# Optimization experiments

Measured on AMD Instinct MI355X. Metric: run time of the kernel, lower is better.

The kernel has to match this reference:

```python
import jax, jax.numpy as jnp
import numpy as np
import math

D_MODEL = 1024
D_ATTN = 128
D_MID = 128
L = 4096

def setup_inputs() -> dict:
    key = jax.random.key(0)
    ks = jax.random.split(key, 5)
    scale = 1.0 / math.sqrt(D_MODEL)
    return {
        "x": jax.random.normal(ks[0], (L, D_MODEL), jnp.float32),
        "z": jax.random.normal(ks[1], (L, D_MODEL), jnp.float32),
        "Wq": jax.random.normal(ks[2], (D_MODEL, D_ATTN), jnp.float32) * scale,
        "bq": jnp.zeros((D_ATTN,), jnp.float32),
        "Wk": jax.random.normal(ks[3], (D_MODEL, D_ATTN), jnp.float32) * scale,
        "bk": jnp.zeros((D_ATTN,), jnp.float32),
        "Wv": jax.random.normal(ks[4], (D_MODEL, D_MID), jnp.float32) * scale,
        "bv": jnp.zeros((D_MID,), jnp.float32),
    }

def reference(x, z, Wq, bq, Wk, bk, Wv, bv):
    # q: [L_x, d_attn], k: [L_z, d_attn], v: [L_z, d_mid]
    q = x @ Wq + bq
    k = z @ Wk + bk
    v = z @ Wv + bv
    inv_sqrt_d = 1.0 / math.sqrt(D_ATTN)
    s = (q @ k.T) * inv_sqrt_d            # [L_x, L_z]
    y = jax.nn.softmax(s, axis=-1) @ v    # [L_x, d_mid]
    return y
```

## Files before the change

kernel.cpp:

```cpp
#include <hip/hip_runtime.h>
#include <hip/hip_bf16.h>

typedef __attribute__((ext_vector_type(8))) short short8;
typedef __attribute__((ext_vector_type(4))) float f32x4;
typedef __attribute__((ext_vector_type(8))) _Float16 half8;

#define L_SEQ 4096
#define DM    1024
#define DA    128
#define AZ    16

#define OFF_QB  786432
#define OFF_KF  1835008
#define OFF_VF  2883584
#define OFF_OA  4063232
#define OA_BYTES ((size_t)AZ * L_SEQ * DA * 2)

__device__ __forceinline__ short f2bf(float f) {
    union { float f; unsigned u; } v; v.f = f;
    unsigned u = v.u;
    u += 0x7FFFu + ((u >> 16) & 1u);
    return (short)(u >> 16);
}

__device__ __forceinline__ unsigned cvt_pk_bf16(float lo, float hi) {
    unsigned r;
    asm("v_cvt_pk_bf16_f32 %0, %1, %2" : "=v"(r) : "v"(lo), "v"(hi));
    return r;
}

typedef const __attribute__((address_space(1))) void g_void_t;
typedef __attribute__((address_space(3))) void l_void_t;
__device__ __forceinline__ void g2lds16(const void* g, void* l) {
    __builtin_amdgcn_global_load_lds((g_void_t*)g, (l_void_t*)l, 16, 0, 0);
}

__global__ __launch_bounds__(256) void prep_w_kernel(
    const float* __restrict__ Wq, const float* __restrict__ Wk,
    const float* __restrict__ Wv, short8* __restrict__ WTf)
{
    const int m = blockIdx.y, kidx = blockIdx.x;
    const float* __restrict__ W = (m == 0) ? Wq : (m == 1) ? Wk : Wv;
    __shared__ __align__(16) float Ws[32 * 132];
    const int t = threadIdx.x;
#pragma unroll
    for (int i = 0; i < 4; i++) {
        const int u = i * 256 + t;
        const int kk = u >> 5, n4 = (u & 31) * 4;
        *(f32x4*)&Ws[kk * 132 + n4] = *(const f32x4*)&W[(size_t)(kidx * 32 + kk) * DA + n4];
    }
    __syncthreads();
#pragma unroll
    for (int i = 0; i < 2; i++) {
        const int u = i * 256 + t;
        const int nt = u >> 6, lane = u & 63, l16 = lane & 15, quad = lane >> 4;
        short8 fr;
#pragma unroll
        for (int j = 0; j < 8; j++)
            fr[j] = f2bf(Ws[(quad * 8 + j) * 132 + nt * 16 + l16]);
        WTf[((size_t)(m * 32 + kidx) * 8 + nt) * 64 + lane] = fr;
    }
}

__global__ __launch_bounds__(256, 1) void qkv_kernel(
    const float* __restrict__ x, const float* __restrict__ z,
    const char* __restrict__ WTraw,
    const float* __restrict__ bq, const float* __restrict__ bk,
    const float* __restrict__ bv,
    short* __restrict__ qb, short8* __restrict__ kf, short8* __restrict__ vf)
{
    __shared__ __align__(16) char smem[2][32768];

    const int t = threadIdx.x;
    const int wave = t >> 6, lane = t & 63;
    const int l16 = lane & 15, quad = lane >> 4;
    const int mtile = wave >> 1, nhalf = wave & 1;
    const int isKV = blockIdx.y;
    const int m1 = isKV ? 1 : 0;
    const int row0 = blockIdx.x * 32;
    const int nbytes = isKV ? 32768 : 16384;

    const float* __restrict__ Am = isKV ? z : x;
    const float* ap = Am + (size_t)(row0 + mtile * 16 + l16) * DM + quad * 8;

    f32x4 acc1[4], acc2[4];
#pragma unroll
    for (int i = 0; i < 4; i++) {
        acc1[i] = (f32x4){0.f, 0.f, 0.f, 0.f};
        acc2[i] = (f32x4){0.f, 0.f, 0.f, 0.f};
    }

    auto stage = [&](int it2, int b) {
        const char* base1 = WTraw + (size_t)(m1 * 32 + it2 * 2) * 8192;
        const char* base2 = WTraw + (size_t)(2 * 32 + it2 * 2) * 8192;
#pragma unroll
        for (int i = 0; i < 8; i++) {
            const int off = i * 4096 + wave * 1024;
            if (off < nbytes) {
                const char* src = (off < 16384) ? (base1 + off) : (base2 + (off - 16384));
                g2lds16(src + lane * 16, &smem[b][off]);
            }
        }
    };

    f32x4 cur[4], nxt[4];
#pragma unroll
    for (int j = 0; j < 2; j++) {
        cur[j * 2]     = *(const f32x4*)(ap + j * 32);
        cur[j * 2 + 1] = *(const f32x4*)(ap + j * 32 + 4);
        nxt[j * 2]     = *(const f32x4*)(ap + 64 + j * 32);
        nxt[j * 2 + 1] = *(const f32x4*)(ap + 64 + j * 32 + 4);
    }

    stage(0, 0);
    __syncthreads();

#pragma unroll 1
    for (int it = 0; it < 16; it++) {
        const int b = it & 1;
        if (it + 1 < 16) stage(it + 1, b ^ 1);

        const int ipf = (it + 2 < 16) ? it + 2 : it;
        f32x4 fut[4];
#pragma unroll
        for (int j = 0; j < 2; j++) {
            fut[j * 2]     = *(const f32x4*)(ap + ipf * 64 + j * 32);
            fut[j * 2 + 1] = *(const f32x4*)(ap + ipf * 64 + j * 32 + 4);
        }

#pragma unroll
        for (int ss = 0; ss < 2; ss++) {
            short8 afr;
#pragma unroll
            for (int j = 0; j < 4; j++) {
                afr[j]     = f2bf(cur[ss * 2][j]);
                afr[4 + j] = f2bf(cur[ss * 2 + 1][j]);
            }
#pragma unroll
            for (int ntl = 0; ntl < 4; ntl++) {
                short8 bfr = *(const short8*)&smem[b][ss * 8192 + ((nhalf * 4 + ntl) * 64 + lane) * 16];
                acc1[ntl] = __builtin_amdgcn_mfma_f32_16x16x32_bf16(afr, bfr, acc1[ntl], 0, 0, 0);
            }
            if (isKV) {
#pragma unroll
                for (int ntl = 0; ntl < 4; ntl++) {
                    short8 bfr = *(const short8*)&smem[b][16384 + ss * 8192 + ((nhalf * 4 + ntl) * 64 + lane) * 16];
                    acc2[ntl] = __builtin_amdgcn_mfma_f32_16x16x32_bf16(afr, bfr, acc2[ntl], 0, 0, 0);
                }
            }
        }
        __syncthreads();
#pragma unroll
        for (int j = 0; j < 4; j++) { cur[j] = nxt[j]; nxt[j] = fut[j]; }
    }

    if (!isKV) {
        const float CL2E = 0.1275187669712930f;
#pragma unroll
        for (int ntl = 0; ntl < 4; ntl++) {
            const int col = nhalf * 64 + ntl * 16 + l16;
            const float bb = bq[col];
#pragma unroll
            for (int r = 0; r < 4; r++)
                qb[(size_t)(row0 + mtile * 16 + quad * 4 + r) * DA + col] =
                    f2bf((acc1[ntl][r] + bb) * CL2E);
        }
        return;
    }

    short* kT = (short*)&smem[0][0];
    short* vT = (short*)&smem[0][16384];
#pragma unroll
    for (int ntl = 0; ntl < 4; ntl++) {
        const int col = nhalf * 64 + ntl * 16 + l16;
        const float bbk = bk[col], bbv = bv[col];
#pragma unroll
        for (int r = 0; r < 4; r++) {
            const int rl = mtile * 16 + quad * 4 + r;
            kT[rl * 132 + col] = f2bf(acc1[ntl][r] + bbk);
            vT[rl * 132 + col] = f2bf(acc2[ntl][r] + bbv);
        }
    }
    __syncthreads();

    const int kg = blockIdx.x;
#pragma unroll
    for (int i = 0; i < 2; i++) {
        const int f = i * 256 + t;
        const int ks = f >> 7, nth = (f >> 6) & 1, ln = f & 63;
        const int lf = ln & 15, qf = ln >> 4;
        short8 fr;
#pragma unroll
        for (int j = 0; j < 8; j++)
            fr[j] = kT[(nth * 16 + lf) * 132 + ks * 32 + qf * 8 + j];
        kf[((size_t)(kg * 4 + ks) * 2 + nth) * 64 + ln] = fr;
    }
#pragma unroll
    for (int i = 0; i < 2; i++) {
        const int f = i * 256 + t;
        const int nt = f >> 6, ln = f & 63;
        const int lf = ln & 15, qf = ln >> 4;
        short8 fr;
#pragma unroll
        for (int j = 0; j < 8; j++)
            fr[j] = vT[(qf * 8 + j) * 132 + nt * 16 + lf];
        vf[((size_t)kg * 8 + nt) * 64 + ln] = fr;
    }
}

__global__ __launch_bounds__(256, 2) void attn_kernel(
    const short* __restrict__ qb, const char* __restrict__ kfg,
    const char* __restrict__ vfg, _Float16* __restrict__ OA,
    float* __restrict__ lA)
{
    __shared__ __align__(16) char kv[2][8192];

    const int t    = threadIdx.x;
    const int wave = t >> 6;
    const int lane = t & 63;
    const int l16  = lane & 15;
    const int quad = lane >> 4;
    const int qr0  = blockIdx.x * 128;
    const int g0   = blockIdx.y * 8;

    auto stage = [&](int g, int b) {
        const char* kb_ = kfg + (size_t)(g0 + g) * 8192 + wave * 2048;
        g2lds16(kb_ + lane * 16,        &kv[b][wave * 2048]);
        g2lds16(kb_ + 1024 + lane * 16, &kv[b][wave * 2048 + 1024]);
    };

    stage(0, 0);

    short8 af[2][4];
#pragma unroll
    for (int mt = 0; mt < 2; mt++) {
        const short* qrow = qb + (size_t)(qr0 + wave * 32 + mt * 16 + l16) * DA + quad * 8;
#pragma unroll
        for (int ks = 0; ks < 4; ks++)
            af[mt][ks] = *(const short8*)(qrow + ks * 32);
    }

    short8 bones;
#pragma unroll
    for (int j = 0; j < 8; j++) bones[j] = (l16 == 0) ? (short)0x3F80 : (short)0;

    f32x4 O[2][9];
#pragma unroll
    for (int mt = 0; mt < 2; mt++)
#pragma unroll
        for (int i = 0; i < 9; i++) O[mt][i] = (f32x4){0.f, 0.f, 0.f, 0.f};

    __syncthreads();

#pragma unroll 1
    for (int g = 0; g < 8; g++) {
        const int b = g & 1;
        if (g + 1 < 8) stage(g + 1, b ^ 1);

        const short8* vgp = (const short8*)(vfg + (size_t)(g0 + g) * 8192);
        short8 b2v[8];
#pragma unroll
        for (int nt = 0; nt < 8; nt++)
            b2v[nt] = vgp[nt * 64 + lane];

        const char* kb_ = &kv[b][0];

        f32x4 st[2][2];
#pragma unroll
        for (int zh = 0; zh < 2; zh++)
#pragma unroll
            for (int mt = 0; mt < 2; mt++) st[zh][mt] = (f32x4){0.f, 0.f, 0.f, 0.f};
        __builtin_amdgcn_s_setprio(1);
#pragma unroll
        for (int ks = 0; ks < 4; ks++)
#pragma unroll
            for (int zh = 0; zh < 2; zh++) {
                const short8 kfr = *(const short8*)(kb_ + ((ks * 2 + zh) * 64 + lane) * 16);
                st[zh][0] = __builtin_amdgcn_mfma_f32_16x16x32_bf16(kfr, af[0][ks], st[zh][0], 0, 0, 0);
                st[zh][1] = __builtin_amdgcn_mfma_f32_16x16x32_bf16(kfr, af[1][ks], st[zh][1], 0, 0, 0);
            }
        __builtin_amdgcn_s_setprio(0);

        short8 a2[2];
#pragma unroll
        for (int mt = 0; mt < 2; mt++) {
            unsigned x0 = cvt_pk_bf16(exp2f(st[0][mt][0]), exp2f(st[0][mt][1]));
            unsigned x1 = cvt_pk_bf16(exp2f(st[0][mt][2]), exp2f(st[0][mt][3]));
            unsigned y0 = cvt_pk_bf16(exp2f(st[1][mt][0]), exp2f(st[1][mt][1]));
            unsigned y1 = cvt_pk_bf16(exp2f(st[1][mt][2]), exp2f(st[1][mt][3]));
            asm volatile("v_permlane32_swap_b32 %0, %1" : "+v"(x0), "+v"(y0));
            asm volatile("v_permlane32_swap_b32 %0, %1" : "+v"(x1), "+v"(y1));
            asm volatile("v_permlane16_swap_b32 %0, %1" : "+v"(x0), "+v"(y0));
            asm volatile("v_permlane16_swap_b32 %0, %1" : "+v"(x1), "+v"(y1));
            union { short8 s; unsigned u[4]; } pa;
            pa.u[0] = x0;
            pa.u[1] = x1;
            pa.u[2] = y0;
            pa.u[3] = y1;
            a2[mt] = pa.s;
        }

        __builtin_amdgcn_s_setprio(1);
#pragma unroll
        for (int nt = 0; nt < 8; nt++) {
            O[0][nt] = __builtin_amdgcn_mfma_f32_16x16x32_bf16(a2[0], b2v[nt], O[0][nt], 0, 0, 0);
            O[1][nt] = __builtin_amdgcn_mfma_f32_16x16x32_bf16(a2[1], b2v[nt], O[1][nt], 0, 0, 0);
        }
        O[0][8] = __builtin_amdgcn_mfma_f32_16x16x32_bf16(a2[0], bones, O[0][8], 0, 0, 0);
        O[1][8] = __builtin_amdgcn_mfma_f32_16x16x32_bf16(a2[1], bones, O[1][8], 0, 0, 0);
        __builtin_amdgcn_s_setprio(0);
        __syncthreads();
    }

    const int rw = qr0 + wave * 32;
    _Float16* Ob = OA + (size_t)blockIdx.y * L_SEQ * DA;
#pragma unroll
    for (int mt = 0; mt < 2; mt++)
#pragma unroll
        for (int nt = 0; nt < 8; nt++)
#pragma unroll
            for (int r = 0; r < 4; r++)
                Ob[(size_t)(rw + mt * 16 + quad * 4 + r) * DA + nt * 16 + l16] =
                    (_Float16)O[mt][nt][r];
    if (l16 == 0) {
        float* lb = lA + (size_t)blockIdx.y * L_SEQ;
#pragma unroll
        for (int mt = 0; mt < 2; mt++)
#pragma unroll
            for (int r = 0; r < 4; r++)
                lb[rw + mt * 16 + quad * 4 + r] = O[mt][8][r];
    }
}

__global__ __launch_bounds__(256) void merge_kernel(
    const _Float16* __restrict__ OA, const float* __restrict__ lA,
    float* __restrict__ out)
{
    const int t = threadIdx.x;
    const int row = blockIdx.x * 16 + (t >> 4);
    const int cg = (t & 15) * 8;

    float acc[8];
#pragma unroll
    for (int j = 0; j < 8; j++) acc[j] = 0.f;
    float lsum = 0.f;
#pragma unroll
    for (int zz = 0; zz < AZ; zz++) {
        const half8 v = *(const half8*)&OA[((size_t)zz * L_SEQ + row) * DA + cg];
#pragma unroll
        for (int j = 0; j < 8; j++) acc[j] += (float)v[j];
        lsum += lA[(size_t)zz * L_SEQ + row];
    }
    const float inv = 1.f / lsum;
    f32x4 o0, o1;
#pragma unroll
    for (int j = 0; j < 4; j++) { o0[j] = acc[j] * inv; o1[j] = acc[4 + j] * inv; }
    f32x4* dst = (f32x4*)&out[(size_t)row * DA + cg];
    dst[0] = o0;
    dst[1] = o1;
}

extern "C" void kernel_launch(void* const* d_in, const int* in_sizes, int n_in,
                              void* d_out, int out_size, void* d_ws, size_t ws_size,
                              hipStream_t stream) {
    (void)in_sizes; (void)n_in; (void)out_size; (void)ws_size;
    const float* x  = (const float*)d_in[0];
    const float* z  = (const float*)d_in[1];
    const float* Wq = (const float*)d_in[2];
    const float* bq = (const float*)d_in[3];
    const float* Wk = (const float*)d_in[4];
    const float* bk = (const float*)d_in[5];
    const float* Wv = (const float*)d_in[6];
    const float* bv = (const float*)d_in[7];
    float* out = (float*)d_out;

    short8*   WTf = (short8*)d_ws;
    short*    qb  = (short*)((char*)d_ws + OFF_QB);
    short8*   kf  = (short8*)((char*)d_ws + OFF_KF);
    short8*   vf  = (short8*)((char*)d_ws + OFF_VF);
    _Float16* OA  = (_Float16*)((char*)d_ws + OFF_OA);
    float*    lA  = (float*)((char*)d_ws + OFF_OA + OA_BYTES);

    prep_w_kernel<<<dim3(32, 3), 256, 0, stream>>>(Wq, Wk, Wv, WTf);
    qkv_kernel<<<dim3(128, 2), 256, 0, stream>>>(x, z, (const char*)WTf,
                                                 bq, bk, bv, qb, kf, vf);
    attn_kernel<<<dim3(32, AZ), 256, 0, stream>>>(qb, (const char*)kf,
                                                  (const char*)vf, OA, lA);
    merge_kernel<<<256, 256, 0, stream>>>(OA, lA, out);
}
```

Baseline: 125.4 us.

## Load K fragments straight to registers and compute softmax row sums on VALU

The attention kernel no longer stages K tiles through double-buffered LDS with a block barrier. Each wave now loads its K fragments directly from global memory into registers, prefetching the next group into a second register set. The extra ones-vector MFMA used for the softmax denominator is replaced by fp32 VALU adds of the exponentials plus two cross-lane shuffles. This removes LDS traffic, __syncthreads, and two MFMAs per iteration, at the cost of more VGPRs and all four waves re-reading the same K data from cache.

```diff
diff --git a/kernel.cpp b/kernel.cpp
--- a/kernel.cpp
+++ b/kernel.cpp
@@ -213,8 +213,6 @@
     const char* __restrict__ vfg, _Float16* __restrict__ OA,
     float* __restrict__ lA)
 {
-    __shared__ __align__(16) char kv[2][8192];
-
     const int t    = threadIdx.x;
     const int wave = t >> 6;
     const int lane = t & 63;
@@ -223,14 +221,6 @@
     const int qr0  = blockIdx.x * 128;
     const int g0   = blockIdx.y * 8;
 
-    auto stage = [&](int g, int b) {
-        const char* kb_ = kfg + (size_t)(g0 + g) * 8192 + wave * 2048;
-        g2lds16(kb_ + lane * 16,        &kv[b][wave * 2048]);
-        g2lds16(kb_ + 1024 + lane * 16, &kv[b][wave * 2048 + 1024]);
-    };
-
-    stage(0, 0);
-
     short8 af[2][4];
 #pragma unroll
     for (int mt = 0; mt < 2; mt++) {
@@ -240,30 +230,33 @@
             af[mt][ks] = *(const short8*)(qrow + ks * 32);
     }
 
-    short8 bones;
-#pragma unroll
-    for (int j = 0; j < 8; j++) bones[j] = (l16 == 0) ? (short)0x3F80 : (short)0;
-
-    f32x4 O[2][9];
+    f32x4 O[2][8];
 #pragma unroll
     for (int mt = 0; mt < 2; mt++)
 #pragma unroll
-        for (int i = 0; i < 9; i++) O[mt][i] = (f32x4){0.f, 0.f, 0.f, 0.f};
-
-    __syncthreads();
+        for (int i = 0; i < 8; i++) O[mt][i] = (f32x4){0.f, 0.f, 0.f, 0.f};
+    float ls[2] = {0.f, 0.f};
+
+    short8 kc[8];
+    {
+        const short8* kgp = (const short8*)(kfg + (size_t)g0 * 8192);
+#pragma unroll
+        for (int i = 0; i < 8; i++) kc[i] = kgp[i * 64 + lane];
+    }
 
 #pragma unroll 1
     for (int g = 0; g < 8; g++) {
-        const int b = g & 1;
-        if (g + 1 < 8) stage(g + 1, b ^ 1);
-
+        short8 kn[8];
+        if (g + 1 < 8) {
+            const short8* kgp = (const short8*)(kfg + (size_t)(g0 + g + 1) * 8192);
+#pragma unroll
+            for (int i = 0; i < 8; i++) kn[i] = kgp[i * 64 + lane];
+        }
         const short8* vgp = (const short8*)(vfg + (size_t)(g0 + g) * 8192);
-        short8 b2v[8];
+        short8 vc[8];
 #pragma unroll
         for (int nt = 0; nt < 8; nt++)
-            b2v[nt] = vgp[nt * 64 + lane];
-
-        const char* kb_ = &kv[b][0];
+            vc[nt] = vgp[nt * 64 + lane];
 
         f32x4 st[2][2];
 #pragma unroll
@@ -275,19 +268,23 @@
         for (int ks = 0; ks < 4; ks++)
 #pragma unroll
             for (int zh = 0; zh < 2; zh++) {
-                const short8 kfr = *(const short8*)(kb_ + ((ks * 2 + zh) * 64 + lane) * 16);
-                st[zh][0] = __builtin_amdgcn_mfma_f32_16x16x32_bf16(kfr, af[0][ks], st[zh][0], 0, 0, 0);
-                st[zh][1] = __builtin_amdgcn_mfma_f32_16x16x32_bf16(kfr, af[1][ks], st[zh][1], 0, 0, 0);
+                st[zh][0] = __builtin_amdgcn_mfma_f32_16x16x32_bf16(kc[ks * 2 + zh], af[0][ks], st[zh][0], 0, 0, 0);
+                st[zh][1] = __builtin_amdgcn_mfma_f32_16x16x32_bf16(kc[ks * 2 + zh], af[1][ks], st[zh][1], 0, 0, 0);
             }
         __builtin_amdgcn_s_setprio(0);
 
         short8 a2[2];
 #pragma unroll
         for (int mt = 0; mt < 2; mt++) {
-            unsigned x0 = cvt_pk_bf16(exp2f(st[0][mt][0]), exp2f(st[0][mt][1]));
-            unsigned x1 = cvt_pk_bf16(exp2f(st[0][mt][2]), exp2f(st[0][mt][3]));
-            unsigned y0 = cvt_pk_bf16(exp2f(st[1][mt][0]), exp2f(st[1][mt][1]));
-            unsigned y1 = cvt_pk_bf16(exp2f(st[1][mt][2]), exp2f(st[1][mt][3]));
+            const float e00 = exp2f(st[0][mt][0]), e01 = exp2f(st[0][mt][1]);
+            const float e02 = exp2f(st[0][mt][2]), e03 = exp2f(st[0][mt][3]);
+            const float e10 = exp2f(st[1][mt][0]), e11 = exp2f(st[1][mt][1]);
+            const float e12 = exp2f(st[1][mt][2]), e13 = exp2f(st[1][mt][3]);
+            ls[mt] += ((e00 + e01) + (e02 + e03)) + ((e10 + e11) + (e12 + e13));
+            unsigned x0 = cvt_pk_bf16(e00, e01);
+            unsigned x1 = cvt_pk_bf16(e02, e03);
+            unsigned y0 = cvt_pk_bf16(e10, e11);
+            unsigned y1 = cvt_pk_bf16(e12, e13);
             asm volatile("v_permlane32_swap_b32 %0, %1" : "+v"(x0), "+v"(y0));
             asm volatile("v_permlane32_swap_b32 %0, %1" : "+v"(x1), "+v"(y1));
             asm volatile("v_permlane16_swap_b32 %0, %1" : "+v"(x0), "+v"(y0));
@@ -303,13 +300,21 @@
         __builtin_amdgcn_s_setprio(1);
 #pragma unroll
         for (int nt = 0; nt < 8; nt++) {
-            O[0][nt] = __builtin_amdgcn_mfma_f32_16x16x32_bf16(a2[0], b2v[nt], O[0][nt], 0, 0, 0);
-            O[1][nt] = __builtin_amdgcn_mfma_f32_16x16x32_bf16(a2[1], b2v[nt], O[1][nt], 0, 0, 0);
-        }
-        O[0][8] = __builtin_amdgcn_mfma_f32_16x16x32_bf16(a2[0], bones, O[0][8], 0, 0, 0);
-        O[1][8] = __builtin_amdgcn_mfma_f32_16x16x32_bf16(a2[1], bones, O[1][8], 0, 0, 0);
+            O[0][nt] = __builtin_amdgcn_mfma_f32_16x16x32_bf16(a2[0], vc[nt], O[0][nt], 0, 0, 0);
+            O[1][nt] = __builtin_amdgcn_mfma_f32_16x16x32_bf16(a2[1], vc[nt], O[1][nt], 0, 0, 0);
+        }
         __builtin_amdgcn_s_setprio(0);
-        __syncthreads();
+
+        if (g + 1 < 8) {
+#pragma unroll
+            for (int i = 0; i < 8; i++) kc[i] = kn[i];
+        }
+    }
+
+#pragma unroll
+    for (int mt = 0; mt < 2; mt++) {
+        ls[mt] += __shfl_xor(ls[mt], 16);
+        ls[mt] += __shfl_xor(ls[mt], 32);
     }
 
     const int rw = qr0 + wave * 32;
@@ -322,13 +327,11 @@
             for (int r = 0; r < 4; r++)
                 Ob[(size_t)(rw + mt * 16 + quad * 4 + r) * DA + nt * 16 + l16] =
                     (_Float16)O[mt][nt][r];
-    if (l16 == 0) {
+    if (quad == 0) {
         float* lb = lA + (size_t)blockIdx.y * L_SEQ;
 #pragma unroll
         for (int mt = 0; mt < 2; mt++)
-#pragma unroll
-            for (int r = 0; r < 4; r++)
-                lb[rw + mt * 16 + quad * 4 + r] = O[mt][8][r];
+            lb[rw + mt * 16 + l16] = ls[mt];
     }
 }
 
```

After: 125.8 us. About the same (+0.4%).
